# Kernel optimization log

Hardware: AMD Instinct MI355X
Metric: run time of the kernel (lower is better)

## Reference

```python
import jax, jax.numpy as jnp
import numpy as np

EMB, HID, V_SRC, V_TGT, NUM_OUT, BOS = 128, 512, 10000, 8000, 9, 0


def _lstm_cell(x, h, c, Wih, Whh, bih, bhh):
    # PyTorch LSTMCell math: gates ordered i, f, g, o
    g = x @ Wih.T + h @ Whh.T + (bih + bhh)
    i, f, gg, o = jnp.split(g, 4, axis=-1)
    i, f, o = jax.nn.sigmoid(i), jax.nn.sigmoid(f), jax.nn.sigmoid(o)
    c = f * c + i * jnp.tanh(gg)
    h = o * jnp.tanh(c)
    return h, c


def setup_inputs() -> dict:
    key = jax.random.key(0)
    ks = jax.random.split(key, 12)
    s = 1.0 / np.sqrt(HID)
    u = lambda k, shp: jax.random.uniform(k, shp, jnp.float32, -s, s)
    src = jax.random.randint(ks[0], (2048, 2), 0, V_SRC)
    src_embed = jax.random.normal(ks[1], (V_SRC, EMB), jnp.float32)
    src_embed = src_embed.at[0].set(0.0)  # padding_idx row
    tgt_embed = jax.random.normal(ks[2], (V_TGT, EMB), jnp.float32)
    tgt_embed = tgt_embed.at[BOS].set(0.0)  # padding_idx=BOS row
    return {
        "src": src,
        "src_embed": src_embed,
        "tgt_embed": tgt_embed,
        "enc_Wih": u(ks[3], (4 * HID, EMB)),
        "enc_Whh": u(ks[4], (4 * HID, HID)),
        "enc_bih": u(ks[5], (4 * HID,)),
        "enc_bhh": u(ks[6], (4 * HID,)),
        "dec_Wih": u(ks[7], (4 * HID, EMB)),
        "dec_Whh": u(ks[8], (4 * HID, HID)),
        "dec_bih": u(ks[9], (4 * HID,)),
        "dec_bhh": u(ks[10], (4 * HID,)),
        "proj_W": u(ks[11], (V_TGT, HID)),
        "proj_b": jnp.zeros((V_TGT,), jnp.float32),
    }


def reference(src, src_embed, tgt_embed, enc_Wih, enc_Whh, enc_bih, enc_bhh,
              dec_Wih, dec_Whh, dec_bih, dec_bhh, proj_W, proj_b):
    B = src.shape[0]
    # ---- encoder over the 2 source tokens ----
    enc_in = src_embed[src]  # (B, 2, EMB); dropout is identity at inference
    h = jnp.zeros((B, HID), jnp.float32)
    c = jnp.zeros((B, HID), jnp.float32)

    def enc_step(carry, x_t):
        h, c = carry
        h, c = _lstm_cell(x_t, h, c, enc_Wih, enc_Whh, enc_bih, enc_bhh)
        return (h, c), None

    (h, c), _ = jax.lax.scan(enc_step, (h, c), jnp.swapaxes(enc_in, 0, 1))

    token0 = jnp.full((B,), BOS, jnp.int32)

    def dec_step(carry, _):
        token, h, c = carry
        x = tgt_embed[token]  # (B, EMB)
        h, c = _lstm_cell(x, h, c, dec_Wih, dec_Whh, dec_bih, dec_bhh)
        logit = h @ proj_W.T + proj_b  # (B, V_TGT)
        nxt = jnp.argmax(logit, axis=-1).astype(jnp.int32)
        return (nxt, h, c), logit

    _, step_logits = jax.lax.scan(dec_step, (token0, h, c), None, length=NUM_OUT)
    # step_logits: (NUM_OUT, B, V_TGT) -> max-pool over steps
    return jnp.max(step_logits, axis=0)
```

## Files before the change

kernel.cpp:

```cpp
#include <hip/hip_runtime.h>
#include <math.h>

#define BB 2048
#define EMB 128
#define HID 512
#define G4 2048
#define VT 8000
#define VTP2 8192
#define NSTEP 9
#define NTILE2 64
#define LDW 132

typedef short bf16x8 __attribute__((ext_vector_type(8)));
typedef float f32x4 __attribute__((ext_vector_type(4)));

__device__ __forceinline__ ushort f2bf(float x) {
    uint u = __float_as_uint(x);
    uint r = (u + 0x7fffu + ((u >> 16) & 1u)) >> 16;
    return (ushort)r;
}
__device__ __forceinline__ float bf2f(ushort h) {
    return __uint_as_float(((uint)h) << 16);
}
__device__ __forceinline__ float sigm(float x) { return 1.0f / (1.0f + expf(-x)); }

__device__ __forceinline__ void gload16(const ushort* g, ushort* l) {
    __builtin_amdgcn_global_load_lds(
        (const __attribute__((address_space(1))) uint*)g,
        (__attribute__((address_space(3))) uint*)l, 16, 0, 0);
}

__device__ __forceinline__ void stage4(
    ushort* Sb,
    const ushort* __restrict__ Ah, const ushort* __restrict__ Al,
    const ushort* __restrict__ Bh, const ushort* __restrict__ Bl,
    int biA, int biB, int K, int k0, int wid, int lane)
{
    const ushort* src = (wid < 2) ? ((wid == 0) ? Ah : Al)
                                  : ((wid == 2) ? Bh : Bl);
    const int rowbase = (wid < 2) ? biA : biB;
    const int rl = lane >> 2, kcp = lane & 3;
    #pragma unroll
    for (int j = 0; j < 8; ++j) {
        int row = j * 16 + rl;
        int kc = (kcp - (row >> 1)) & 3;
        const ushort* g = src + (size_t)(rowbase + row) * K + k0 + kc * 8;
        gload16(g, Sb + wid * 4096 + j * 512);
    }
}

__device__ __forceinline__ void stage8(
    ushort* Sb,
    const ushort* __restrict__ Ah, const ushort* __restrict__ Al,
    const ushort* __restrict__ Bh, const ushort* __restrict__ Bl,
    int biA, int biB, int K, int k0, int wid, int lane)
{
    const int rl = lane >> 2, kcp = lane & 3;
    #pragma unroll
    for (int j = 0; j < 4; ++j) {
        int c = wid * 4 + j;
        int region = c >> 3;
        int rowblk = c & 7;
        int row = rowblk * 16 + rl;
        int kc = (kcp - (row >> 1)) & 3;
        const ushort* src = (region < 2) ? (region == 0 ? Ah : Al)
                                         : (region == 2 ? Bh : Bl);
        int base = (region < 2) ? biA : biB;
        gload16(src + (size_t)(base + row) * K + k0 + kc * 8,
                Sb + region * 4096 + rowblk * 512);
    }
}

__global__ __launch_bounds__(64) void gather2_kernel(
    ushort* __restrict__ Xhi, ushort* __restrict__ Xlo,
    const float* __restrict__ table,
    const int* __restrict__ src, int mode, int offset,
    const float* __restrict__ partval, const int* __restrict__ partidx)
{
    int row = blockIdx.x, t = threadIdx.x;
    int tok;
    if (mode == 0) {
        tok = src[row * 2 + offset];
    } else if (mode == 1) {
        tok = 0;
    } else {
        float v = partval[(size_t)row * NTILE2 + t];
        int  ix = partidx[(size_t)row * NTILE2 + t];
        #pragma unroll
        for (int off = 1; off < 64; off <<= 1) {
            float ov = __shfl_xor(v, off, 64);
            int   oi = __shfl_xor(ix, off, 64);
            if (ov > v || (ov == v && oi < ix)) { v = ov; ix = oi; }
        }
        tok = ix;
    }
    float2 e = *(const float2*)&table[(size_t)tok * EMB + t * 2];
    ushort2 hh, hl;
    hh.x = f2bf(e.x); hl.x = f2bf(e.x - bf2f(hh.x));
    hh.y = f2bf(e.y); hl.y = f2bf(e.y - bf2f(hh.y));
    *(ushort2*)&Xhi[row * EMB + t * 2] = hh;
    *(ushort2*)&Xlo[row * EMB + t * 2] = hl;
}

__global__ __launch_bounds__(256) void convgate_kernel(
    const float* __restrict__ W, ushort* __restrict__ Whi, ushort* __restrict__ Wlo,
    int kshift)
{
    size_t e0 = ((size_t)blockIdx.x * 256 + threadIdx.x) * 8;
    int K = 1 << kshift;
    int in_row = (int)(e0 >> kshift);
    int q = in_row & 511, gate = in_row >> 9;
    size_t o0 = (((size_t)(q * 4 + gate)) << kshift) + (e0 & (K - 1));
    float4 v0 = *(const float4*)&W[e0];
    float4 v1 = *(const float4*)&W[e0 + 4];
    float x[8] = {v0.x, v0.y, v0.z, v0.w, v1.x, v1.y, v1.z, v1.w};
    uint p[4], qq[4];
    #pragma unroll
    for (int j = 0; j < 4; ++j) {
        ushort h0 = f2bf(x[2 * j]),     l0 = f2bf(x[2 * j] - bf2f(h0));
        ushort h1 = f2bf(x[2 * j + 1]), l1 = f2bf(x[2 * j + 1] - bf2f(h1));
        p[j]  = (uint)h0 | ((uint)h1 << 16);
        qq[j] = (uint)l0 | ((uint)l1 << 16);
    }
    *(uint4*)&Whi[o0] = make_uint4(p[0], p[1], p[2], p[3]);
    *(uint4*)&Wlo[o0] = make_uint4(qq[0], qq[1], qq[2], qq[3]);
}

__global__ __launch_bounds__(256) void convgbias_kernel(
    const float* __restrict__ b0, const float* __restrict__ b1, float* __restrict__ bp)
{
    int i = blockIdx.x * 256 + threadIdx.x;
    int q = i >> 2, gate = i & 3;
    bp[i] = b0[gate * 512 + q] + b1[gate * 512 + q];
}

__global__ __launch_bounds__(256) void convw_kernel(
    const float* __restrict__ W, ushort* __restrict__ Whi, ushort* __restrict__ Wlo)
{
    size_t e0 = ((size_t)blockIdx.x * 256 + threadIdx.x) * 8;
    int row = (int)(e0 >> 9);
    uint p[4], q[4];
    if (row < VT) {
        float4 v0 = *(const float4*)&W[e0];
        float4 v1 = *(const float4*)&W[e0 + 4];
        float x[8] = {v0.x, v0.y, v0.z, v0.w, v1.x, v1.y, v1.z, v1.w};
        #pragma unroll
        for (int j = 0; j < 4; ++j) {
            ushort h0 = f2bf(x[2 * j]),     l0 = f2bf(x[2 * j] - bf2f(h0));
            ushort h1 = f2bf(x[2 * j + 1]), l1 = f2bf(x[2 * j + 1] - bf2f(h1));
            p[j] = (uint)h0 | ((uint)h1 << 16);
            q[j] = (uint)l0 | ((uint)l1 << 16);
        }
    } else {
        #pragma unroll
        for (int j = 0; j < 4; ++j) { p[j] = 0u; q[j] = 0u; }
    }
    *(uint4*)&Whi[e0] = make_uint4(p[0], p[1], p[2], p[3]);
    *(uint4*)&Wlo[e0] = make_uint4(q[0], q[1], q[2], q[3]);
}

__global__ __launch_bounds__(256) void convb_kernel(
    const float* __restrict__ b, float* __restrict__ bp)
{
    int i = blockIdx.x * 256 + threadIdx.x;
    if (i < VTP2) bp[i] = (i < VT) ? b[i] : -1e30f;
}

__global__ __launch_bounds__(512) void gatescell_kernel(
    const ushort* __restrict__ Xhi, const ushort* __restrict__ Xlo,
    const ushort* __restrict__ Hhi, const ushort* __restrict__ Hlo,
    const ushort* __restrict__ WihH, const ushort* __restrict__ WihL,
    const ushort* __restrict__ WhhH, const ushort* __restrict__ WhhL,
    const float* __restrict__ bperm,
    float* __restrict__ Cst,
    ushort* __restrict__ OHhi, ushort* __restrict__ OHlo,
    int nk)
{
    __shared__ __align__(16) char smem[128 * LDW * 4];
    ushort* S0 = (ushort*)smem;

    const int t = threadIdx.x;
    const int n = blockIdx.x;
    const int tile = (n & 7) * 2 + ((n >> 3) & 1);
    const int rb = n >> 4;
    const int bj0 = tile * 128;
    const int bi0 = rb * 128;
    const int il = t & 15;
    const int g  = (t >> 4) & 3;
    const int wid = t >> 6;
    const int lane = t & 63;
    const int wr = wid >> 2;
    const int wc = wid & 3;

    int aofs[4], bofs[2];
    #pragma unroll
    for (int m = 0; m < 4; ++m) {
        int r = wr * 64 + m * 16 + il;
        aofs[m] = r * 32 + (((g + (r >> 1)) & 3) << 3);
    }
    #pragma unroll
    for (int nn = 0; nn < 2; ++nn) {
        int r = wc * 32 + nn * 16 + il;
        bofs[nn] = 8192 + r * 32 + (((g + (r >> 1)) & 3) << 3);
    }

    f32x4 acc[4][2];
    #pragma unroll
    for (int m = 0; m < 4; ++m)
        #pragma unroll
        for (int nn = 0; nn < 2; ++nn) acc[m][nn] = 0.0f;

    stage8(S0, Xhi, Xlo, WihH, WihL, bi0, bj0, EMB, 0, wid, lane);
    __syncthreads();

    for (int ks = 0; ks < nk; ++ks) {
        int cur = ks & 1;
        if (ks + 1 < nk) {
            int kn = ks + 1;
            if (kn < 4) stage8(S0 + (cur ^ 1) * 16384, Xhi, Xlo, WihH, WihL, bi0, bj0, EMB, kn * 32, wid, lane);
            else        stage8(S0 + (cur ^ 1) * 16384, Hhi, Hlo, WhhH, WhhL, bi0, bj0, HID, (kn - 4) * 32, wid, lane);
        }
        ushort* Sb = S0 + cur * 16384;
        bf16x8 ah[4], al[4];
        #pragma unroll
        for (int m = 0; m < 4; ++m) {
            ah[m] = *(const bf16x8*)&Sb[aofs[m]];
            al[m] = *(const bf16x8*)&Sb[4096 + aofs[m]];
        }
        #pragma unroll
        for (int nn = 0; nn < 2; ++nn) {
            bf16x8 bh = *(const bf16x8*)&Sb[bofs[nn]];
            bf16x8 bl = *(const bf16x8*)&Sb[4096 + bofs[nn]];
            #pragma unroll
            for (int m = 0; m < 4; ++m) {
                acc[m][nn] = __builtin_amdgcn_mfma_f32_16x16x32_bf16(ah[m], bh, acc[m][nn], 0, 0, 0);
                acc[m][nn] = __builtin_amdgcn_mfma_f32_16x16x32_bf16(ah[m], bl, acc[m][nn], 0, 0, 0);
                acc[m][nn] = __builtin_amdgcn_mfma_f32_16x16x32_bf16(al[m], bh, acc[m][nn], 0, 0, 0);
            }
        }
        __syncthreads();
    }

    float* Tr = (float*)smem;
    float bn[2];
    #pragma unroll
    for (int nn = 0; nn < 2; ++nn) bn[nn] = bperm[bj0 + wc * 32 + nn * 16 + il];

    #pragma unroll
    for (int m = 0; m < 4; ++m)
        #pragma unroll
        for (int nn = 0; nn < 2; ++nn)
            #pragma unroll
            for (int j = 0; j < 4; ++j)
                Tr[(wr * 64 + m * 16 + g * 4 + j) * LDW + wc * 32 + nn * 16 + il]
                    = acc[m][nn][j] + bn[nn];
    __syncthreads();

    #pragma unroll
    for (int it = 0; it < 8; ++it) {
        int row = it * 16 + (t >> 5);
        int c4 = t & 31;
        float4 gv = *(float4*)&Tr[row * LDW + c4 * 4];
        float gi = sigm(gv.x), gf = sigm(gv.y), gg = tanhf(gv.z), go = sigm(gv.w);
        size_t o = (size_t)(bi0 + row) * HID + (bj0 >> 2) + c4;
        float cnew = gf * Cst[o] + gi * gg;
        float h = go * tanhf(cnew);
        Cst[o] = cnew;
        ushort hh = f2bf(h);
        OHhi[o] = hh;
        OHlo[o] = f2bf(h - bf2f(hh));
    }
}

__global__ __launch_bounds__(256) void proj_kernel(
    const ushort* __restrict__ Ahi, const ushort* __restrict__ Alo,
    const ushort* __restrict__ Whi, const ushort* __restrict__ Wlo,
    const float* __restrict__ biasp,
    float* __restrict__ outmax,
    float* __restrict__ partval, int* __restrict__ partidx,
    int mode)
{
    __shared__ __align__(16) char smem[128 * LDW * 4];
    ushort* S0 = (ushort*)smem;

    const int t = threadIdx.x;
    const int n = blockIdx.x;
    const int xcd = n & 7;
    const int j8 = n >> 3;
    const int tile = xcd * 8 + (j8 & 7);
    const int rb = j8 >> 3;
    const int bj0 = tile * 128;
    const int bi0 = rb * 128;
    const int il = t & 15;
    const int g  = (t >> 4) & 3;
    const int wid = t >> 6;
    const int lane = t & 63;
    const int wr = wid >> 1, wc = wid & 1;

    int aofs[4], bofs[4];
    #pragma unroll
    for (int m = 0; m < 4; ++m) {
        int r = wr * 64 + m * 16 + il;
        aofs[m] = r * 32 + (((g + (r >> 1)) & 3) << 3);
    }
    #pragma unroll
    for (int nn = 0; nn < 4; ++nn) {
        int r = wc * 64 + nn * 16 + il;
        bofs[nn] = 8192 + r * 32 + (((g + (r >> 1)) & 3) << 3);
    }

    f32x4 acc[4][4];
    #pragma unroll
    for (int m = 0; m < 4; ++m)
        #pragma unroll
        for (int nn = 0; nn < 4; ++nn) acc[m][nn] = 0.0f;

    stage4(S0, Ahi, Alo, Whi, Wlo, bi0, bj0, HID, 0, wid, lane);
    __syncthreads();

    for (int ks = 0; ks < 16; ++ks) {
        int cur = ks & 1;
        if (ks + 1 < 16)
            stage4(S0 + (cur ^ 1) * 16384, Ahi, Alo, Whi, Wlo, bi0, bj0, HID, (ks + 1) * 32, wid, lane);
        ushort* Sb = S0 + cur * 16384;
        bf16x8 ah[4], al[4];
        #pragma unroll
        for (int m = 0; m < 4; ++m) {
            ah[m] = *(const bf16x8*)&Sb[aofs[m]];
            al[m] = *(const bf16x8*)&Sb[4096 + aofs[m]];
        }
        #pragma unroll
        for (int nn = 0; nn < 4; ++nn) {
            bf16x8 bh = *(const bf16x8*)&Sb[bofs[nn]];
            bf16x8 bl = *(const bf16x8*)&Sb[4096 + bofs[nn]];
            #pragma unroll
            for (int m = 0; m < 4; ++m) {
                acc[m][nn] = __builtin_amdgcn_mfma_f32_16x16x32_bf16(ah[m], bh, acc[m][nn], 0, 0, 0);
                acc[m][nn] = __builtin_amdgcn_mfma_f32_16x16x32_bf16(ah[m], bl, acc[m][nn], 0, 0, 0);
                acc[m][nn] = __builtin_amdgcn_mfma_f32_16x16x32_bf16(al[m], bh, acc[m][nn], 0, 0, 0);
            }
        }
        __syncthreads();
    }

    float* Tr = (float*)smem;
    float bn[4];
    #pragma unroll
    for (int nn = 0; nn < 4; ++nn) bn[nn] = biasp[bj0 + wc * 64 + nn * 16 + il];

    #pragma unroll
    for (int m = 0; m < 4; ++m)
        #pragma unroll
        for (int nn = 0; nn < 4; ++nn)
            #pragma unroll
            for (int j = 0; j < 4; ++j)
                Tr[(wr * 64 + m * 16 + g * 4 + j) * LDW + wc * 64 + nn * 16 + il]
                    = acc[m][nn][j] + bn[nn];
    __syncthreads();

    #pragma unroll
    for (int it = 0; it < 16; ++it) {
        int row2 = it * 8 + (t >> 5);
        int c4 = t & 31;
        int row = bi0 + row2;
        int col = bj0 + c4 * 4;
        float4 cur = *(float4*)&Tr[row2 * LDW + c4 * 4];

        float bv = cur.x; int bix = col;
        if (cur.y > bv) { bv = cur.y; bix = col + 1; }
        if (cur.z > bv) { bv = cur.z; bix = col + 2; }
        if (cur.w > bv) { bv = cur.w; bix = col + 3; }
        #pragma unroll
        for (int off = 1; off < 32; off <<= 1) {
            float ov = __shfl_xor(bv, off, 64);
            int   oi = __shfl_xor(bix, off, 64);
            if (ov > bv || (ov == bv && oi < bix)) { bv = ov; bix = oi; }
        }
        if ((t & 31) == 0) {
            partval[(size_t)row * NTILE2 + tile] = bv;
            partidx[(size_t)row * NTILE2 + tile] = bix;
        }

        if (col < VT) {
            float* op = &outmax[(size_t)row * VT + col];
            float4 o = cur;
            if (mode == 2) {
                float4 p = *(const float4*)op;
                o.x = fmaxf(o.x, p.x); o.y = fmaxf(o.y, p.y);
                o.z = fmaxf(o.z, p.z); o.w = fmaxf(o.w, p.w);
            }
            *(float4*)op = o;
        }
    }
}

extern "C" void kernel_launch(void* const* d_in, const int* in_sizes, int n_in,
                              void* d_out, int out_size, void* d_ws, size_t ws_size,
                              hipStream_t stream) {
    const int*   src       = (const int*)d_in[0];
    const float* src_embed = (const float*)d_in[1];
    const float* tgt_embed = (const float*)d_in[2];
    const float* enc_Wih   = (const float*)d_in[3];
    const float* enc_Whh   = (const float*)d_in[4];
    const float* enc_bih   = (const float*)d_in[5];
    const float* enc_bhh   = (const float*)d_in[6];
    const float* dec_Wih   = (const float*)d_in[7];
    const float* dec_Whh   = (const float*)d_in[8];
    const float* dec_bih   = (const float*)d_in[9];
    const float* dec_bhh   = (const float*)d_in[10];
    const float* proj_W    = (const float*)d_in[11];
    const float* proj_b    = (const float*)d_in[12];
    float* out = (float*)d_out;

    char* ws = (char*)d_ws;
    float*  C     = (float*)ws;   ws += (size_t)BB * HID * 4;
    float*  PV    = (float*)ws;   ws += (size_t)BB * NTILE2 * 4;
    int*    PI    = (int*)ws;     ws += (size_t)BB * NTILE2 * 4;
    ushort* Xhi   = (ushort*)ws;  ws += (size_t)BB * EMB * 2;
    ushort* Xlo   = (ushort*)ws;  ws += (size_t)BB * EMB * 2;
    ushort* Hhi   = (ushort*)ws;  ws += (size_t)BB * HID * 2;
    ushort* Hlo   = (ushort*)ws;  ws += (size_t)BB * HID * 2;
    ushort* PWhi  = (ushort*)ws;  ws += (size_t)VTP2 * HID * 2;
    ushort* PWlo  = (ushort*)ws;  ws += (size_t)VTP2 * HID * 2;
    float*  biasp = (float*)ws;   ws += (size_t)VTP2 * 4;
    ushort* eWihH = (ushort*)ws;  ws += (size_t)G4 * EMB * 2;
    ushort* eWihL = (ushort*)ws;  ws += (size_t)G4 * EMB * 2;
    ushort* eWhhH = (ushort*)ws;  ws += (size_t)G4 * HID * 2;
    ushort* eWhhL = (ushort*)ws;  ws += (size_t)G4 * HID * 2;
    ushort* dWihH = (ushort*)ws;  ws += (size_t)G4 * EMB * 2;
    ushort* dWihL = (ushort*)ws;  ws += (size_t)G4 * EMB * 2;
    ushort* dWhhH = (ushort*)ws;  ws += (size_t)G4 * HID * 2;
    ushort* dWhhL = (ushort*)ws;  ws += (size_t)G4 * HID * 2;
    float*  BSe   = (float*)ws;   ws += (size_t)G4 * 4;
    float*  BSd   = (float*)ws;   ws += (size_t)G4 * 4;

    hipMemsetAsync(C, 0, (size_t)BB * HID * 4, stream);

    convw_kernel<<<VTP2 * HID / 8 / 256, 256, 0, stream>>>(proj_W, PWhi, PWlo);
    convb_kernel<<<VTP2 / 256, 256, 0, stream>>>(proj_b, biasp);
    convgate_kernel<<<G4 * EMB / 8 / 256, 256, 0, stream>>>(enc_Wih, eWihH, eWihL, 7);
    convgate_kernel<<<G4 * HID / 8 / 256, 256, 0, stream>>>(enc_Whh, eWhhH, eWhhL, 9);
    convgate_kernel<<<G4 * EMB / 8 / 256, 256, 0, stream>>>(dec_Wih, dWihH, dWihL, 7);
    convgate_kernel<<<G4 * HID / 8 / 256, 256, 0, stream>>>(dec_Whh, dWhhH, dWhhL, 9);
    convgbias_kernel<<<G4 / 256, 256, 0, stream>>>(enc_bih, enc_bhh, BSe);
    convgbias_kernel<<<G4 / 256, 256, 0, stream>>>(dec_bih, dec_bhh, BSd);

    for (int tstep = 0; tstep < 2; ++tstep) {
        gather2_kernel<<<BB, 64, 0, stream>>>(Xhi, Xlo, src_embed, src, 0, tstep, PV, PI);
        gatescell_kernel<<<256, 512, 0, stream>>>(Xhi, Xlo, Hhi, Hlo,
            eWihH, eWihL, eWhhH, eWhhL, BSe, C, Hhi, Hlo, tstep == 0 ? 4 : 20);
    }

    for (int s = 0; s < NSTEP; ++s) {
        gather2_kernel<<<BB, 64, 0, stream>>>(Xhi, Xlo, tgt_embed, nullptr,
            (s == 0 ? 1 : 2), 0, PV, PI);
        gatescell_kernel<<<256, 512, 0, stream>>>(Xhi, Xlo, Hhi, Hlo,
            dWihH, dWihL, dWhhH, dWhhL, BSd, C, Hhi, Hlo, 20);
        proj_kernel<<<1024, 256, 0, stream>>>(Hhi, Hlo, PWhi, PWlo, biasp,
            out, PV, PI, (s == 0 ? 1 : 2));
    }
}
```

Measured before the change: 1.089 ms.

## Overlap LDS staging with MFMA via partial vmcnt waits and prefetch outmax

Both GEMM loops now use raw s_barrier with partial s_waitcnt vmcnt counts instead of __syncthreads. This keeps the next K-slice's global loads in flight while the current slice is consumed, removing the full drain at each barrier. The projection kernel also loads the previous running-max values into registers at kernel start, so that read latency is hidden behind the GEMM. The risks are that the hard-coded vmcnt counts assume exact load counts per stage, the 16 extra float4 registers add register pressure, and the prefetch reads padded columns past VT without a bounds check.

```diff
diff --git a/kernel.cpp b/kernel.cpp
--- a/kernel.cpp
+++ b/kernel.cpp
@@ -211,7 +211,6 @@
         for (int nn = 0; nn < 2; ++nn) acc[m][nn] = 0.0f;
 
     stage8(S0, Xhi, Xlo, WihH, WihL, bi0, bj0, EMB, 0, wid, lane);
-    __syncthreads();
 
     for (int ks = 0; ks < nk; ++ks) {
         int cur = ks & 1;
@@ -220,6 +219,11 @@
             if (kn < 4) stage8(S0 + (cur ^ 1) * 16384, Xhi, Xlo, WihH, WihL, bi0, bj0, EMB, kn * 32, wid, lane);
             else        stage8(S0 + (cur ^ 1) * 16384, Hhi, Hlo, WhhH, WhhL, bi0, bj0, HID, (kn - 4) * 32, wid, lane);
         }
+        if (ks + 1 < nk) asm volatile("s_waitcnt vmcnt(4)" ::: "memory");
+        else             asm volatile("s_waitcnt vmcnt(0)" ::: "memory");
+        __builtin_amdgcn_s_barrier();
+        __builtin_amdgcn_sched_barrier(0);
+
         ushort* Sb = S0 + cur * 16384;
         bf16x8 ah[4], al[4];
         #pragma unroll
@@ -238,7 +242,9 @@
                 acc[m][nn] = __builtin_amdgcn_mfma_f32_16x16x32_bf16(al[m], bh, acc[m][nn], 0, 0, 0);
             }
         }
-        __syncthreads();
+        __builtin_amdgcn_sched_barrier(0);
+        __builtin_amdgcn_s_barrier();
+        __builtin_amdgcn_sched_barrier(0);
     }
 
     float* Tr = (float*)smem;
@@ -297,6 +303,16 @@
     const int lane = t & 63;
     const int wr = wid >> 1, wc = wid & 1;
 
+    float4 oldv[16];
+    const bool rmw = (mode == 2);
+    if (rmw) {
+        #pragma unroll
+        for (int it = 0; it < 16; ++it) {
+            int row2 = it * 8 + (t >> 5);
+            oldv[it] = *(const float4*)&outmax[(size_t)(bi0 + row2) * VT + bj0 + (t & 31) * 4];
+        }
+    }
+
     int aofs[4], bofs[4];
     #pragma unroll
     for (int m = 0; m < 4; ++m) {
@@ -316,12 +332,16 @@
         for (int nn = 0; nn < 4; ++nn) acc[m][nn] = 0.0f;
 
     stage4(S0, Ahi, Alo, Whi, Wlo, bi0, bj0, HID, 0, wid, lane);
-    __syncthreads();
 
     for (int ks = 0; ks < 16; ++ks) {
         int cur = ks & 1;
         if (ks + 1 < 16)
             stage4(S0 + (cur ^ 1) * 16384, Ahi, Alo, Whi, Wlo, bi0, bj0, HID, (ks + 1) * 32, wid, lane);
+        if (ks + 1 < 16) asm volatile("s_waitcnt vmcnt(8)" ::: "memory");
+        else             asm volatile("s_waitcnt vmcnt(0)" ::: "memory");
+        __builtin_amdgcn_s_barrier();
+        __builtin_amdgcn_sched_barrier(0);
+
         ushort* Sb = S0 + cur * 16384;
         bf16x8 ah[4], al[4];
         #pragma unroll
@@ -340,7 +360,9 @@
                 acc[m][nn] = __builtin_amdgcn_mfma_f32_16x16x32_bf16(al[m], bh, acc[m][nn], 0, 0, 0);
             }
         }
-        __syncthreads();
+        __builtin_amdgcn_sched_barrier(0);
+        __builtin_amdgcn_s_barrier();
+        __builtin_amdgcn_sched_barrier(0);
     }
 
     float* Tr = (float*)smem;
@@ -382,14 +404,13 @@
         }
 
         if (col < VT) {
-            float* op = &outmax[(size_t)row * VT + col];
             float4 o = cur;
-            if (mode == 2) {
-                float4 p = *(const float4*)op;
+            if (rmw) {
+                float4 p = oldv[it];
                 o.x = fmaxf(o.x, p.x); o.y = fmaxf(o.y, p.y);
                 o.z = fmaxf(o.z, p.z); o.w = fmaxf(o.w, p.w);
             }
-            *(float4*)op = o;
+            *(float4*)&outmax[(size_t)row * VT + col] = o;
         }
     }
 }
```

Result: faster. 1.043 ms (-4.2%).
